# Performance work log

Measured on AMD Instinct MI355X. Metric: run time of the kernel, lower is better.

Reference implementation:

```python
import jax, jax.numpy as jnp
import numpy as np

N_WIRES = 4
N_LAYERS = 2
DIM = 2 ** N_WIRES  # 16
# sign of PauliZ on wire w for basis state i (wire 0 = most significant bit)
_SIGNS = np.array([[1.0 - 2.0 * ((i >> (N_WIRES - 1 - w)) & 1) for w in range(N_WIRES)]
                   for i in range(DIM)], dtype=np.float32)  # (16, 4)


def _apply_1q(state, gate, wire):
    """state: (N,2,2,2,2) complex; gate: (2,2) shared or (N,2,2) batched."""
    s = jnp.moveaxis(state, wire + 1, -1)
    if gate.ndim == 3:
        s = jnp.einsum('nab,n...b->n...a', gate, s)
    else:
        s = jnp.einsum('ab,n...b->n...a', gate, s)
    return jnp.moveaxis(s, -1, wire + 1)


def _apply_cnot(state, ctrl, tgt):
    s = jnp.moveaxis(state, (ctrl + 1, tgt + 1), (-2, -1))
    s = s.at[..., 1, :].set(s[..., 1, ::-1])  # flip target where control=1
    return jnp.moveaxis(s, (-2, -1), (ctrl + 1, tgt + 1))


def _ry(t):  # t: scalar or (N,) -> (2,2) or (N,2,2)
    c, s = jnp.cos(t / 2), jnp.sin(t / 2)
    m = jnp.stack([jnp.stack([c, -s], -1), jnp.stack([s, c], -1)], -2)
    return m.astype(jnp.complex64)


def _rx(t):
    c = jnp.cos(t / 2).astype(jnp.complex64)
    s = jnp.sin(t / 2).astype(jnp.complex64)
    return jnp.stack([jnp.stack([c, -1j * s], -1), jnp.stack([-1j * s, c], -1)], -2)


def _rz(t):
    em = jnp.exp(-0.5j * t)
    ep = jnp.exp(0.5j * t)
    z = jnp.zeros_like(em)
    return jnp.stack([jnp.stack([em, z], -1), jnp.stack([z, ep], -1)], -2).astype(jnp.complex64)


def _simulate(angles, params):
    """angles: (N,4) RY encoding angles; params: (L,4,3). Returns (N,4) <Z_w>."""
    N = angles.shape[0]
    state = jnp.zeros((N, 2, 2, 2, 2), jnp.complex64).at[:, 0, 0, 0, 0].set(1.0)
    for w in range(N_WIRES):
        state = _apply_1q(state, _ry(angles[:, w]), w)
    for l in range(N_LAYERS):
        for w in range(N_WIRES):
            state = _apply_1q(state, _rx(params[l, w, 0]), w)
            state = _apply_1q(state, _ry(params[l, w, 1]), w)
            state = _apply_1q(state, _rz(params[l, w, 2]), w)
        for w in range(N_WIRES - 1):
            state = _apply_cnot(state, w, w + 1)
        state = _apply_cnot(state, N_WIRES - 1, 0)
    probs = (state.real ** 2 + state.imag ** 2).reshape(N, DIM)
    return probs @ jnp.asarray(_SIGNS)  # (N, 4)


def setup_inputs() -> dict:
    key = jax.random.key(0)
    kx, kp = jax.random.split(key)
    x = jax.random.uniform(kx, (1024, 1, 28, 28), dtype=jnp.float32)
    params = jax.random.normal(kp, (N_LAYERS, N_WIRES, 3), dtype=jnp.float32)
    return {"x": x, "params": params}


def reference(x, params):
    B = x.shape[0]
    # extract 2x2 patches in (r, c) raster order, flattened row-major -> (B*196, 4)
    patches = x[:, 0].reshape(B, 14, 2, 14, 2).transpose(0, 1, 3, 2, 4).reshape(B * 196, 4)
    ev = _simulate(patches, params)          # (B*196, 4)
    return ev.reshape(B, 196 * N_WIRES)       # (B, 784)
```

## Files before the change

### kernel.cpp

```cpp
#include <hip/hip_runtime.h>

struct cplx { float x, y; };

__device__ __forceinline__ cplx cmul(cplx a, cplx b) {
    cplx r;
    r.x = fmaf(a.x, b.x, -(a.y * b.y));
    r.y = fmaf(a.x, b.y,  a.y * b.x);
    return r;
}

__device__ __forceinline__ cplx cmadd2(cplx u0, cplx a0, cplx u1, cplx a1) {
    cplx r;
    r.x = fmaf(u0.x, a0.x, -(u0.y * a0.y)) + fmaf(u1.x, a1.x, -(u1.y * a1.y));
    r.y = fmaf(u0.x, a0.y,  u0.y * a0.x)  + fmaf(u1.x, a1.y,  u1.y * a1.x);
    return r;
}

__global__ __launch_bounds__(256) void quanv_kernel(const float* __restrict__ x,
                                                    const float* __restrict__ prm,
                                                    float* __restrict__ out,
                                                    int n) {
    int t = blockIdx.x * blockDim.x + threadIdx.x;
    if (t >= n) return;

    int b  = t / 196;
    int pi = t - b * 196;
    int r  = pi / 14;
    int c  = pi - r * 14;

    const float* xb = x + b * 784 + r * 56 + c * 2;
    float2 top = *(const float2*)(xb);
    float2 bot = *(const float2*)(xb + 28);
    float ang[4] = { top.x, top.y, bot.x, bot.y };

    float cw[4], sw[4];
#pragma unroll
    for (int w = 0; w < 4; ++w) __sincosf(0.5f * ang[w], &sw[w], &cw[w]);

    cplx st[16];
#pragma unroll
    for (int i = 0; i < 16; ++i) {
        float a = ((i & 8) ? sw[0] : cw[0]) * ((i & 4) ? sw[1] : cw[1])
                * ((i & 2) ? sw[2] : cw[2]) * ((i & 1) ? sw[3] : cw[3]);
        st[i].x = a; st[i].y = 0.0f;
    }

#pragma unroll
    for (int l = 0; l < 2; ++l) {
#pragma unroll
        for (int w = 0; w < 4; ++w) {
            float sa, ca, sb, cb, sc, cc;
            __sincosf(0.5f * prm[(l * 4 + w) * 3 + 0], &sa, &ca);
            __sincosf(0.5f * prm[(l * 4 + w) * 3 + 1], &sb, &cb);
            __sincosf(0.5f * prm[(l * 4 + w) * 3 + 2], &sc, &cc);
            cplx m00 = {  cb * ca,  sb * sa };
            cplx m01 = { -sb * ca, -cb * sa };
            cplx m10 = {  sb * ca, -cb * sa };
            cplx m11 = {  cb * ca, -sb * sa };
            cplx em = { cc, -sc }, ep = { cc, sc };
            cplx u00 = cmul(em, m00), u01 = cmul(em, m01);
            cplx u10 = cmul(ep, m10), u11 = cmul(ep, m11);

            int strd = 8 >> w;
#pragma unroll
            for (int i = 0; i < 16; ++i) {
                if (i & strd) continue;
                cplx a0 = st[i], a1 = st[i + strd];
                st[i]        = cmadd2(u00, a0, u01, a1);
                st[i + strd] = cmadd2(u10, a0, u11, a1);
            }
        }
#pragma unroll
        for (int w = 0; w < 4; ++w) {
            int ctrl = w, tgt = (w + 1) & 3;
            int scm = 8 >> ctrl, stm = 8 >> tgt;
#pragma unroll
            for (int i = 0; i < 16; ++i) {
                if ((i & scm) && !(i & stm)) {
                    cplx tmp = st[i]; st[i] = st[i | stm]; st[i | stm] = tmp;
                }
            }
        }
    }

    float ev0 = 0.f, ev1 = 0.f, ev2 = 0.f, ev3 = 0.f;
#pragma unroll
    for (int i = 0; i < 16; ++i) {
        float p2 = fmaf(st[i].x, st[i].x, st[i].y * st[i].y);
        ev0 += (i & 8) ? -p2 : p2;
        ev1 += (i & 4) ? -p2 : p2;
        ev2 += (i & 2) ? -p2 : p2;
        ev3 += (i & 1) ? -p2 : p2;
    }
    float4 o = { ev0, ev1, ev2, ev3 };
    *(float4*)(out + t * 4) = o;
}

extern "C" void kernel_launch(void* const* d_in, const int* in_sizes, int n_in,
                              void* d_out, int out_size, void* d_ws, size_t ws_size,
                              hipStream_t stream) {
    const float* x   = (const float*)d_in[0];
    const float* prm = (const float*)d_in[1];
    float* out = (float*)d_out;

    int B = in_sizes[0] / 784;
    int n = B * 196;
    int block = 256;
    int grid = (n + block - 1) / block;
    quanv_kernel<<<grid, block, 0, stream>>>(x, prm, out, n);
}
```

Baseline: 63.56 us.

## Precompute fused gate matrices and exploit product-state structure for first layer

A tiny preliminary kernel now computes the eight fused RZ·RY·RX 2x2 unitaries once, so the main kernel no longer runs per-thread sincos for them. The main kernel also folds the RY encoding and the first layer's rotations into per-wire 2-vectors, because the state is still a product state at that point, and builds the 16-amplitude state with tensor products. This removes the first layer's dense gate application. The expectation-value reduction is restructured as a butterfly of partial sums. The cost is an extra kernel launch and workspace traffic, plus the gate loads in every thread.

```diff
diff --git a/kernel.cpp b/kernel.cpp
--- a/kernel.cpp
+++ b/kernel.cpp
@@ -16,8 +16,27 @@
     return r;
 }
 
+__global__ void prep_gates(const float* __restrict__ prm, float* __restrict__ g) {
+    int k = threadIdx.x;
+    if (k >= 8) return;
+    float sa, ca, sb, cb, sc, cc;
+    __sincosf(0.5f * prm[k * 3 + 0], &sa, &ca);
+    __sincosf(0.5f * prm[k * 3 + 1], &sb, &cb);
+    __sincosf(0.5f * prm[k * 3 + 2], &sc, &cc);
+    cplx m00 = {  cb * ca,  sb * sa };
+    cplx m01 = { -sb * ca, -cb * sa };
+    cplx m10 = {  sb * ca, -cb * sa };
+    cplx m11 = {  cb * ca, -sb * sa };
+    cplx em = { cc, -sc }, ep = { cc, sc };
+    cplx u00 = cmul(em, m00), u01 = cmul(em, m01);
+    cplx u10 = cmul(ep, m10), u11 = cmul(ep, m11);
+    float* o = g + k * 8;
+    o[0] = u00.x; o[1] = u00.y; o[2] = u01.x; o[3] = u01.y;
+    o[4] = u10.x; o[5] = u10.y; o[6] = u11.x; o[7] = u11.y;
+}
+
 __global__ __launch_bounds__(256) void quanv_kernel(const float* __restrict__ x,
-                                                    const float* __restrict__ prm,
+                                                    const float* __restrict__ g,
                                                     float* __restrict__ out,
                                                     int n) {
     int t = blockIdx.x * blockDim.x + threadIdx.x;
@@ -33,67 +52,87 @@
     float2 bot = *(const float2*)(xb + 28);
     float ang[4] = { top.x, top.y, bot.x, bot.y };
 
-    float cw[4], sw[4];
+    cplx U[8][4];
 #pragma unroll
-    for (int w = 0; w < 4; ++w) __sincosf(0.5f * ang[w], &sw[w], &cw[w]);
-
-    cplx st[16];
-#pragma unroll
-    for (int i = 0; i < 16; ++i) {
-        float a = ((i & 8) ? sw[0] : cw[0]) * ((i & 4) ? sw[1] : cw[1])
-                * ((i & 2) ? sw[2] : cw[2]) * ((i & 1) ? sw[3] : cw[3]);
-        st[i].x = a; st[i].y = 0.0f;
+    for (int k = 0; k < 8; ++k) {
+        const float* o = g + k * 8;
+        U[k][0] = { o[0], o[1] };
+        U[k][1] = { o[2], o[3] };
+        U[k][2] = { o[4], o[5] };
+        U[k][3] = { o[6], o[7] };
     }
 
+    cplx v[4][2];
 #pragma unroll
-    for (int l = 0; l < 2; ++l) {
+    for (int w = 0; w < 4; ++w) {
+        float cw, sw;
+        __sincosf(0.5f * ang[w], &sw, &cw);
+        v[w][0].x = fmaf(cw, U[w][0].x, sw * U[w][1].x);
+        v[w][0].y = fmaf(cw, U[w][0].y, sw * U[w][1].y);
+        v[w][1].x = fmaf(cw, U[w][2].x, sw * U[w][3].x);
+        v[w][1].y = fmaf(cw, U[w][2].y, sw * U[w][3].y);
+    }
+
+    cplx p01[4], p23[4], st[16];
 #pragma unroll
-        for (int w = 0; w < 4; ++w) {
-            float sa, ca, sb, cb, sc, cc;
-            __sincosf(0.5f * prm[(l * 4 + w) * 3 + 0], &sa, &ca);
-            __sincosf(0.5f * prm[(l * 4 + w) * 3 + 1], &sb, &cb);
-            __sincosf(0.5f * prm[(l * 4 + w) * 3 + 2], &sc, &cc);
-            cplx m00 = {  cb * ca,  sb * sa };
-            cplx m01 = { -sb * ca, -cb * sa };
-            cplx m10 = {  sb * ca, -cb * sa };
-            cplx m11 = {  cb * ca, -sb * sa };
-            cplx em = { cc, -sc }, ep = { cc, sc };
-            cplx u00 = cmul(em, m00), u01 = cmul(em, m01);
-            cplx u10 = cmul(ep, m10), u11 = cmul(ep, m11);
+    for (int j = 0; j < 4; ++j) {
+        p01[j] = cmul(v[0][j >> 1], v[1][j & 1]);
+        p23[j] = cmul(v[2][j >> 1], v[3][j & 1]);
+    }
+#pragma unroll
+    for (int i = 0; i < 16; ++i) st[i] = cmul(p01[i >> 2], p23[i & 3]);
 
-            int strd = 8 >> w;
 #pragma unroll
-            for (int i = 0; i < 16; ++i) {
-                if (i & strd) continue;
-                cplx a0 = st[i], a1 = st[i + strd];
-                st[i]        = cmadd2(u00, a0, u01, a1);
-                st[i + strd] = cmadd2(u10, a0, u11, a1);
-            }
-        }
+    for (int w = 0; w < 4; ++w) {
+        int scm = 8 >> w, stm = 8 >> ((w + 1) & 3);
 #pragma unroll
-        for (int w = 0; w < 4; ++w) {
-            int ctrl = w, tgt = (w + 1) & 3;
-            int scm = 8 >> ctrl, stm = 8 >> tgt;
-#pragma unroll
-            for (int i = 0; i < 16; ++i) {
-                if ((i & scm) && !(i & stm)) {
-                    cplx tmp = st[i]; st[i] = st[i | stm]; st[i | stm] = tmp;
-                }
+        for (int i = 0; i < 16; ++i) {
+            if ((i & scm) && !(i & stm)) {
+                cplx tmp = st[i]; st[i] = st[i | stm]; st[i | stm] = tmp;
             }
         }
     }
 
-    float ev0 = 0.f, ev1 = 0.f, ev2 = 0.f, ev3 = 0.f;
 #pragma unroll
-    for (int i = 0; i < 16; ++i) {
-        float p2 = fmaf(st[i].x, st[i].x, st[i].y * st[i].y);
-        ev0 += (i & 8) ? -p2 : p2;
-        ev1 += (i & 4) ? -p2 : p2;
-        ev2 += (i & 2) ? -p2 : p2;
-        ev3 += (i & 1) ? -p2 : p2;
+    for (int w = 0; w < 4; ++w) {
+        cplx u00 = U[4 + w][0], u01 = U[4 + w][1];
+        cplx u10 = U[4 + w][2], u11 = U[4 + w][3];
+        int strd = 8 >> w;
+#pragma unroll
+        for (int i = 0; i < 16; ++i) {
+            if (i & strd) continue;
+            cplx a0 = st[i], a1 = st[i + strd];
+            st[i]        = cmadd2(u00, a0, u01, a1);
+            st[i + strd] = cmadd2(u10, a0, u11, a1);
+        }
     }
-    float4 o = { ev0, ev1, ev2, ev3 };
-    *(float4*)(out + t * 4) = o;
+
+#pragma unroll
+    for (int w = 0; w < 4; ++w) {
+        int scm = 8 >> w, stm = 8 >> ((w + 1) & 3);
+#pragma unroll
+        for (int i = 0; i < 16; ++i) {
+            if ((i & scm) && !(i & stm)) {
+                cplx tmp = st[i]; st[i] = st[i | stm]; st[i | stm] = tmp;
+            }
+        }
+    }
+
+    float p[16];
+#pragma unroll
+    for (int i = 0; i < 16; ++i) p[i] = fmaf(st[i].x, st[i].x, st[i].y * st[i].y);
+
+    float a[8], ev3 = 0.f;
+#pragma unroll
+    for (int i = 0; i < 8; ++i) { a[i] = p[2*i] + p[2*i+1]; ev3 += p[2*i] - p[2*i+1]; }
+    float bs[4], ev2 = 0.f;
+#pragma unroll
+    for (int i = 0; i < 4; ++i) { bs[i] = a[2*i] + a[2*i+1]; ev2 += a[2*i] - a[2*i+1]; }
+    float ev1 = (bs[0] - bs[1]) + (bs[2] - bs[3]);
+    float ev0 = (bs[0] + bs[1]) - (bs[2] + bs[3]);
+
+    float4 o4 = { ev0, ev1, ev2, ev3 };
+    *(float4*)(out + t * 4) = o4;
 }
 
 extern "C" void kernel_launch(void* const* d_in, const int* in_sizes, int n_in,
@@ -102,10 +141,13 @@
     const float* x   = (const float*)d_in[0];
     const float* prm = (const float*)d_in[1];
     float* out = (float*)d_out;
+    float* gates = (float*)d_ws;
 
     int B = in_sizes[0] / 784;
     int n = B * 196;
+
+    prep_gates<<<1, 64, 0, stream>>>(prm, gates);
     int block = 256;
     int grid = (n + block - 1) / block;
-    quanv_kernel<<<grid, block, 0, stream>>>(x, prm, out, n);
+    quanv_kernel<<<grid, block, 0, stream>>>(x, gates, out, n);
 }
```

New measurement: 62.13 us. -2.3%, faster.

## Precompute gate matrices in shared memory and fold first layer into product state

Applied to the files above, without the earlier changes.

Eight threads per block compute the fused RX·RY·RZ unitaries once and store them in shared memory, so each thread no longer evaluates 24 sincos calls. Before any CNOT the state is a product state, so the first layer's gates are applied to each single-qubit RY-encoded vector and combined by tensor product. The first CNOT ring is absorbed as a fixed index permutation. The second CNOT ring is folded into the measurement signs through a butterfly reduction over the probabilities. This removes most per-thread trig and gate arithmetic, at the cost of a block-level barrier and shared-memory reads.

```diff
diff --git a/kernel.cpp b/kernel.cpp
--- a/kernel.cpp
+++ b/kernel.cpp
@@ -20,7 +20,27 @@
                                                     const float* __restrict__ prm,
                                                     float* __restrict__ out,
                                                     int n) {
-    int t = blockIdx.x * blockDim.x + threadIdx.x;
+    __shared__ float gs[64];
+    int tid = threadIdx.x;
+    if (tid < 8) {
+        float sa, ca, sb, cb, sc, cc;
+        __sincosf(0.5f * prm[tid * 3 + 0], &sa, &ca);
+        __sincosf(0.5f * prm[tid * 3 + 1], &sb, &cb);
+        __sincosf(0.5f * prm[tid * 3 + 2], &sc, &cc);
+        cplx m00 = {  cb * ca,  sb * sa };
+        cplx m01 = { -sb * ca, -cb * sa };
+        cplx m10 = {  sb * ca, -cb * sa };
+        cplx m11 = {  cb * ca, -sb * sa };
+        cplx em = { cc, -sc }, ep = { cc, sc };
+        cplx u00 = cmul(em, m00), u01 = cmul(em, m01);
+        cplx u10 = cmul(ep, m10), u11 = cmul(ep, m11);
+        float* o = gs + tid * 8;
+        o[0] = u00.x; o[1] = u00.y; o[2] = u01.x; o[3] = u01.y;
+        o[4] = u10.x; o[5] = u10.y; o[6] = u11.x; o[7] = u11.y;
+    }
+    __syncthreads();
+
+    int t = blockIdx.x * 256 + tid;
     if (t >= n) return;
 
     int b  = t / 196;
@@ -33,67 +53,71 @@
     float2 bot = *(const float2*)(xb + 28);
     float ang[4] = { top.x, top.y, bot.x, bot.y };
 
-    float cw[4], sw[4];
+    cplx v[4][2];
 #pragma unroll
-    for (int w = 0; w < 4; ++w) __sincosf(0.5f * ang[w], &sw[w], &cw[w]);
+    for (int w = 0; w < 4; ++w) {
+        float cw, sw;
+        __sincosf(0.5f * ang[w], &sw, &cw);
+        const float* o = gs + w * 8;
+        v[w][0].x = fmaf(cw, o[0], sw * o[2]);
+        v[w][0].y = fmaf(cw, o[1], sw * o[3]);
+        v[w][1].x = fmaf(cw, o[4], sw * o[6]);
+        v[w][1].y = fmaf(cw, o[5], sw * o[7]);
+    }
 
-    cplx st[16];
+    cplx p01[4], p23[4], st[16];
 #pragma unroll
-    for (int i = 0; i < 16; ++i) {
-        float a = ((i & 8) ? sw[0] : cw[0]) * ((i & 4) ? sw[1] : cw[1])
-                * ((i & 2) ? sw[2] : cw[2]) * ((i & 1) ? sw[3] : cw[3]);
-        st[i].x = a; st[i].y = 0.0f;
+    for (int j = 0; j < 4; ++j) {
+        p01[j] = cmul(v[0][j >> 1], v[1][j & 1]);
+        p23[j] = cmul(v[2][j >> 1], v[3][j & 1]);
+    }
+#pragma unroll
+    for (int j = 0; j < 16; ++j) {
+        int w0 = (j >> 3) & 1, w1 = (j >> 2) & 1, w2 = (j >> 1) & 1, w3 = j & 1;
+        int n1 = w1 ^ w0;
+        int n2 = w2 ^ w1 ^ w0;
+        int n3 = w3 ^ w2 ^ w1 ^ w0;
+        int n0 = w3 ^ w2 ^ w1;
+        int pj = (n0 << 3) | (n1 << 2) | (n2 << 1) | n3;
+        st[pj] = cmul(p01[j >> 2], p23[j & 3]);
     }
 
 #pragma unroll
-    for (int l = 0; l < 2; ++l) {
+    for (int w = 0; w < 4; ++w) {
+        const float* o = gs + (4 + w) * 8;
+        cplx u00 = { o[0], o[1] }, u01 = { o[2], o[3] };
+        cplx u10 = { o[4], o[5] }, u11 = { o[6], o[7] };
+        int strd = 8 >> w;
 #pragma unroll
-        for (int w = 0; w < 4; ++w) {
-            float sa, ca, sb, cb, sc, cc;
-            __sincosf(0.5f * prm[(l * 4 + w) * 3 + 0], &sa, &ca);
-            __sincosf(0.5f * prm[(l * 4 + w) * 3 + 1], &sb, &cb);
-            __sincosf(0.5f * prm[(l * 4 + w) * 3 + 2], &sc, &cc);
-            cplx m00 = {  cb * ca,  sb * sa };
-            cplx m01 = { -sb * ca, -cb * sa };
-            cplx m10 = {  sb * ca, -cb * sa };
-            cplx m11 = {  cb * ca, -sb * sa };
-            cplx em = { cc, -sc }, ep = { cc, sc };
-            cplx u00 = cmul(em, m00), u01 = cmul(em, m01);
-            cplx u10 = cmul(ep, m10), u11 = cmul(ep, m11);
-
-            int strd = 8 >> w;
-#pragma unroll
-            for (int i = 0; i < 16; ++i) {
-                if (i & strd) continue;
-                cplx a0 = st[i], a1 = st[i + strd];
-                st[i]        = cmadd2(u00, a0, u01, a1);
-                st[i + strd] = cmadd2(u10, a0, u11, a1);
-            }
-        }
-#pragma unroll
-        for (int w = 0; w < 4; ++w) {
-            int ctrl = w, tgt = (w + 1) & 3;
-            int scm = 8 >> ctrl, stm = 8 >> tgt;
-#pragma unroll
-            for (int i = 0; i < 16; ++i) {
-                if ((i & scm) && !(i & stm)) {
-                    cplx tmp = st[i]; st[i] = st[i | stm]; st[i | stm] = tmp;
-                }
-            }
+        for (int i = 0; i < 16; ++i) {
+            if (i & strd) continue;
+            cplx a0 = st[i], a1 = st[i + strd];
+            st[i]        = cmadd2(u00, a0, u01, a1);
+            st[i + strd] = cmadd2(u10, a0, u11, a1);
         }
     }
 
-    float ev0 = 0.f, ev1 = 0.f, ev2 = 0.f, ev3 = 0.f;
+    float p[16];
 #pragma unroll
-    for (int i = 0; i < 16; ++i) {
-        float p2 = fmaf(st[i].x, st[i].x, st[i].y * st[i].y);
-        ev0 += (i & 8) ? -p2 : p2;
-        ev1 += (i & 4) ? -p2 : p2;
-        ev2 += (i & 2) ? -p2 : p2;
-        ev3 += (i & 1) ? -p2 : p2;
+    for (int i = 0; i < 16; ++i) p[i] = fmaf(st[i].x, st[i].x, st[i].y * st[i].y);
+
+    float as[8], ad[8];
+#pragma unroll
+    for (int i = 0; i < 8; ++i) { as[i] = p[2*i] + p[2*i+1]; ad[i] = p[2*i] - p[2*i+1]; }
+    float bss[4], bsd[4], bdd[4];
+#pragma unroll
+    for (int i = 0; i < 4; ++i) {
+        bss[i] = as[2*i] + as[2*i+1];
+        bsd[i] = as[2*i] - as[2*i+1];
+        bdd[i] = ad[2*i] - ad[2*i+1];
     }
-    float4 o = { ev0, ev1, ev2, ev3 };
-    *(float4*)(out + t * 4) = o;
+    float ev1 = (bss[0] - bss[1]) - (bss[2] - bss[3]);
+    float ev2 = (bsd[0] - bsd[1]) - (bsd[2] - bsd[3]);
+    float ev0 = (bdd[0] - bdd[1]) + (bdd[2] - bdd[3]);
+    float ev3 = (bdd[0] - bdd[1]) - (bdd[2] - bdd[3]);
+
+    float4 o4 = { ev0, ev1, ev2, ev3 };
+    *(float4*)(out + t * 4) = o4;
 }
 
 extern "C" void kernel_launch(void* const* d_in, const int* in_sizes, int n_in,
```

Result: faster. 60.15 us (-5.4%).
